# Optimization experiments

Measured on AMD Instinct MI355X. Metric: run time of the kernel, lower is better.

The kernel has to match this reference:

```python
import jax, jax.numpy as jnp
import numpy as np

B, N, H, D, T = 2, 512, 128, 128, 8  # batch, nodes, feat width, mid/out size, triplet fts
Z = 2 * H  # concat(node_fts, hidden)


def _lin_params(key, fan_in, fan_out):
    kw, kb = jax.random.split(key)
    scale = 1.0 / np.sqrt(fan_in)
    w = jax.random.uniform(kw, (fan_in, fan_out), jnp.float32, -scale, scale)
    b = jax.random.uniform(kb, (fan_out,), jnp.float32, -scale, scale)
    return w, b


def setup_inputs() -> dict:
    key = jax.random.key(0)
    ks = jax.random.split(key, 16)
    inp = {
        'node_fts': jax.random.normal(ks[0], (B, N, H), jnp.float32),
        'edge_fts': jax.random.normal(ks[1], (B, N, N, H), jnp.float32),
        'graph_fts': jax.random.normal(ks[2], (B, H), jnp.float32),
        'adj_mat': (jax.random.uniform(ks[3], (B, N, N)) < 0.5).astype(jnp.float32),
        'hidden': jax.random.normal(ks[4], (B, N, H), jnp.float32),
    }
    # message linears
    inp['Wm1'], inp['bm1'] = _lin_params(ks[5], Z, D)
    inp['Wm2'], inp['bm2'] = _lin_params(ks[6], Z, D)
    inp['Wme'], inp['bme'] = _lin_params(ks[7], H, D)
    inp['Wmg'], inp['bmg'] = _lin_params(ks[8], H, D)
    # output linears
    inp['Wo1'], inp['bo1'] = _lin_params(ks[9], Z, D)
    inp['Wo2'], inp['bo2'] = _lin_params(ks[10], D, D)
    # triplet linears
    inp['Wt1'], inp['bt1'] = _lin_params(ks[11], Z, T)
    inp['Wt2'], inp['bt2'] = _lin_params(ks[12], Z, T)
    inp['Wte'], inp['bte'] = _lin_params(ks[13], H, T)
    inp['Wtg'], inp['btg'] = _lin_params(ks[14], H, T)
    return inp


def reference(node_fts, edge_fts, graph_fts, adj_mat, hidden,
              Wm1, bm1, Wm2, bm2, Wme, bme, Wmg, bmg,
              Wo1, bo1, Wo2, bo2,
              Wt1, bt1, Wt2, bt2, Wte, bte, Wtg, btg):
    z = jnp.concatenate([node_fts, hidden], axis=-1)  # [b,n,2h]

    msg_1 = z @ Wm1 + bm1            # [b,n,d]
    msg_2 = z @ Wm2 + bm2            # [b,n,d]
    msg_e = edge_fts @ Wme + bme     # [b,n,n,d]
    msg_g = graph_fts @ Wmg + bmg    # [b,d]

    # triplet messages: broadcast pairwise sum -> relu, shape [b,n,n,t]
    tri = (z @ Wt1 + bt1)[:, None, :, :] \
        + (z @ Wt2 + bt2)[:, :, None, :] \
        + (edge_fts @ Wte + bte) \
        + (graph_fts @ Wtg + btg)[:, None, None, :]
    tri_msgs = jax.nn.relu(tri)

    # pairwise message broadcast-add, mask by adjacency, max over senders (axis 1)
    msgs = msg_1[:, None, :, :] + msg_2[:, :, None, :] + msg_e \
         + msg_g[:, None, None, :]                      # [b,n,n,d]
    msgs = jnp.max(msgs * adj_mat[..., None], axis=1)   # [b,n,d]

    ret = (z @ Wo1 + bo1) + (msgs @ Wo2 + bo2)           # [b,n,d]
    return (ret, tri_msgs)
```

## Files before the change

### kernel.cpp

```cpp
#include <hip/hip_runtime.h>
#include <hip/hip_bf16.h>

#define NB 2
#define NN 512
#define HH 128
#define DD 128
#define TT 8

#define WPACK_OFF 0
#define C_OFF     36864
#define BROW_OFF  561152
#define TC_OFF    1085440
#define TB_OFF    1118208
#define OC_OFF    1150976
#define PART_OFF  1675264
#define ZF_OFF    18452480

#define OUT_TRI   131072

typedef float f32x4 __attribute__((ext_vector_type(4)));
typedef short s16x8 __attribute__((ext_vector_type(8)));

__device__ __forceinline__ unsigned short f2bf(float f) {
    union { float f; unsigned int u; } x; x.f = f;
    unsigned int u = x.u;
    unsigned int r = (u + 0x7FFFu + ((u >> 16) & 1u)) >> 16;
    return (unsigned short)r;
}

__global__ __launch_bounds__(256) void k0_precompute(
    const float* __restrict__ node, const float* __restrict__ hidden,
    const float* __restrict__ graph,
    const float* __restrict__ Wm1, const float* __restrict__ Wm2,
    const float* __restrict__ Wo1, const float* __restrict__ Wmg,
    const float* __restrict__ Wt1, const float* __restrict__ Wt2,
    const float* __restrict__ Wtg,
    const float* __restrict__ Wme, const float* __restrict__ Wte,
    const float* __restrict__ bm1, const float* __restrict__ bm2,
    const float* __restrict__ bme, const float* __restrict__ bmg,
    const float* __restrict__ bo1, const float* __restrict__ bo2,
    const float* __restrict__ bt1, const float* __restrict__ bt2,
    const float* __restrict__ bte, const float* __restrict__ btg,
    char* __restrict__ ws)
{
    const int bx = blockIdx.x, tid = threadIdx.x;
    if (bx == 256) {
        unsigned short* wp = (unsigned short*)(ws + WPACK_OFF);
        for (int idx = tid; idx < 16 * 144 * 8; idx += 256) {
            int j = idx & 7, tmp = idx >> 3;
            int n = tmp % 144, kq = tmp / 144;
            int k = kq * 8 + j;
            float v = 0.f;
            if (n < 128) v = Wme[k * 128 + n];
            else if (n < 136) v = Wte[k * 8 + (n - 128)];
            wp[idx] = f2bf(v);
        }
        return;
    }
    __shared__ float zs[4 * 257];
    const int row0 = bx * 4;
    const int b = row0 >> 9;
    #pragma unroll
    for (int e = 0; e < 4; e++) {
        int idx = e * 256 + tid;
        int rl = idx >> 8, col = idx & 255;
        float v = (col < 128) ? node[(row0 + rl) * 128 + col]
                              : hidden[(row0 + rl) * 128 + col - 128];
        zs[rl * 257 + col] = v;
    }
    __syncthreads();

    float* Cws = (float*)(ws + C_OFF);
    float* Bws = (float*)(ws + BROW_OFF);
    float* Ows = (float*)(ws + OC_OFF);
    float* TCw = (float*)(ws + TC_OFF);
    float* TBw = (float*)(ws + TB_OFF);

    const int d = tid & 127, half = tid >> 7;
    const float* z0 = zs + (half * 2) * 257;
    const float* z1 = zs + (half * 2 + 1) * 257;
    float c0 = 0.f, c1 = 0.f, q0 = 0.f, q1 = 0.f, o0 = 0.f, o1 = 0.f;
    for (int k = 0; k < 256; k++) {
        float w1 = Wm1[k * 128 + d], w2 = Wm2[k * 128 + d], wo = Wo1[k * 128 + d];
        float za = z0[k], zb = z1[k];
        c0 += za * w1; c1 += zb * w1;
        q0 += za * w2; q1 += zb * w2;
        o0 += za * wo; o1 += zb * wo;
    }
    float gm = 0.f;
    for (int k = 0; k < 128; k++) gm += graph[b * 128 + k] * Wmg[k * 128 + d];
    const float cb = gm + bm1[d] + bm2[d] + bme[d] + bmg[d];
    const float ob = bo1[d] + bo2[d];
    const int r0 = row0 + half * 2;
    Cws[r0 * 128 + d] = c0 + cb;  Cws[(r0 + 1) * 128 + d] = c1 + cb;
    Bws[r0 * 128 + d] = q0;       Bws[(r0 + 1) * 128 + d] = q1;
    Ows[r0 * 128 + d] = o0 + ob;  Ows[(r0 + 1) * 128 + d] = o1 + ob;

    if (tid < 64) {
        int r4 = tid >> 4, t = (tid >> 1) & 7, which = tid & 1;
        const float* zr = zs + r4 * 257;
        const float* W = which ? Wt2 : Wt1;
        float acc = 0.f;
        for (int k = 0; k < 256; k++) acc += zr[k] * W[k * 8 + t];
        int rg = row0 + r4;
        if (which == 0) {
            float gt = 0.f;
            for (int k = 0; k < 128; k++) gt += graph[b * 128 + k] * Wtg[k * 8 + t];
            TCw[rg * 8 + t] = acc + gt + bt1[t] + bt2[t] + bte[t] + btg[t];
        } else {
            TBw[rg * 8 + t] = acc;
        }
    }
}

__global__ __launch_bounds__(512, 2) void k2_main(
    const float* __restrict__ edge, const float* __restrict__ adj,
    char* __restrict__ ws, float* __restrict__ out)
{
    __shared__ float red[8][16][64];
    __shared__ int zflag[16];
    const int tid = threadIdx.x;
    const int jt = blockIdx.x, ic = blockIdx.y, b = blockIdx.z;
    const int j0 = jt * 16, i0 = ic * 64;

    const int lane = tid & 63, wave = tid >> 6;
    const int g = wave >> 2, sq = wave & 3;
    const int quad = lane >> 4, l15 = lane & 15;
    const int ntbase = g * 4;

    if (tid < 16) zflag[tid] = 0;
    __syncthreads();

    const float* Bws = (const float*)(ws + BROW_OFF);
    const float* TCw = (const float*)(ws + TC_OFF);
    const float* TBw = (const float*)(ws + TB_OFF);
    const s16x8* wp8 = (const s16x8*)(ws + WPACK_OFF);
    float* part = (float*)(ws + PART_OFF);
    int* Zws = (int*)(ws + ZF_OFF);

    s16x8 Bf[5][4];
    #pragma unroll
    for (int s = 0; s < 4; s++) {
        #pragma unroll
        for (int ntl = 0; ntl < 5; ntl++) {
            int nt = (ntl < 4) ? (ntbase + ntl) : 8;
            Bf[ntl][s] = wp8[(4 * s + quad) * 144 + nt * 16 + l15];
        }
    }

    const int jb = j0 + quad * 4;
    float TCf[4];
    #pragma unroll
    for (int r = 0; r < 4; r++)
        TCf[r] = (l15 < 8) ? TCw[(b * 512 + jb + r) * 8 + l15] : 0.f;

    float Mx[4][4];
    #pragma unroll
    for (int ntl = 0; ntl < 4; ntl++)
        #pragma unroll
        for (int r = 0; r < 4; r++) Mx[ntl][r] = -INFINITY;
    int anyz[4] = {0, 0, 0, 0};

    for (int ii = 0; ii < 16; ii++) {
        const int ig = i0 + sq * 16 + ii;
        const float* erow = edge + ((b * 512 + ig) * 512 + j0 + l15) * 128 + quad * 8;
        s16x8 af[4];
        #pragma unroll
        for (int s = 0; s < 4; s++) {
            float4 p = *(const float4*)(erow + s * 32);
            float4 q = *(const float4*)(erow + s * 32 + 4);
            s16x8 a;
            a[0] = (short)f2bf(p.x); a[1] = (short)f2bf(p.y);
            a[2] = (short)f2bf(p.z); a[3] = (short)f2bf(p.w);
            a[4] = (short)f2bf(q.x); a[5] = (short)f2bf(q.y);
            a[6] = (short)f2bf(q.z); a[7] = (short)f2bf(q.w);
            af[s] = a;
        }
        float adjv[4];
        const int arow = (b * 512 + ig) * 512 + jb;
        #pragma unroll
        for (int r = 0; r < 4; r++) adjv[r] = adj[arow + r];
        float brw[4];
        const int br0 = (b * 512 + ig) * 128;
        #pragma unroll
        for (int ntl = 0; ntl < 4; ntl++)
            brw[ntl] = Bws[br0 + (ntbase + ntl) * 16 + l15];
        const float tb = (l15 < 8) ? TBw[(b * 512 + ig) * 8 + l15] : 0.f;

        f32x4 acc[5];
        #pragma unroll
        for (int ntl = 0; ntl < 5; ntl++) acc[ntl] = (f32x4){0.f, 0.f, 0.f, 0.f};
        #pragma unroll
        for (int s = 0; s < 4; s++) {
            #pragma unroll
            for (int ntl = 0; ntl < 5; ntl++)
                acc[ntl] = __builtin_amdgcn_mfma_f32_16x16x32_bf16(
                    af[s], Bf[ntl][s], acc[ntl], 0, 0, 0);
        }
        #pragma unroll
        for (int r = 0; r < 4; r++) {
            const int isz = (adjv[r] == 0.f);
            anyz[r] |= isz;
            #pragma unroll
            for (int ntl = 0; ntl < 4; ntl++) {
                float v = isz ? -INFINITY : (acc[ntl][r] + brw[ntl]);
                Mx[ntl][r] = fmaxf(Mx[ntl][r], v);
            }
        }
        if (g == 1 && l15 < 8) {
            float* tout = out + OUT_TRI + ((b * 512 + ig) * 512 + jb) * 8 + l15;
            #pragma unroll
            for (int r = 0; r < 4; r++) {
                float tv = acc[4][r] + TCf[r] + tb;
                tout[r * 8] = fmaxf(tv, 0.f);
            }
        }
        if ((ii & 3) == 3) __syncthreads();
    }

    if (g == 0 && l15 == 0) {
        #pragma unroll
        for (int r = 0; r < 4; r++)
            if (anyz[r]) atomicOr(&zflag[quad * 4 + r], 1);
    }
    #pragma unroll
    for (int ntl = 0; ntl < 4; ntl++)
        #pragma unroll
        for (int r = 0; r < 4; r++)
            red[wave][quad * 4 + r][ntl * 16 + l15] = Mx[ntl][r];
    __syncthreads();

    {
        const int q = tid;
        const int j = q >> 5, dq = q & 31;
        const int g2 = dq >> 4, c0 = (dq & 15) * 4;
        const float* r0p = &red[g2 * 4][j][c0];
        float4 m = *(const float4*)r0p;
        #pragma unroll
        for (int w = 1; w < 4; w++) {
            const float4 o = *(const float4*)&red[g2 * 4 + w][j][c0];
            m.x = fmaxf(m.x, o.x); m.y = fmaxf(m.y, o.y);
            m.z = fmaxf(m.z, o.z); m.w = fmaxf(m.w, o.w);
        }
        *(float4*)(part + ((b * 8 + ic) * 512 + j0 + j) * 128 + dq * 4) = m;
    }
    if (tid < 16) Zws[(b * 8 + ic) * 512 + j0 + tid] = zflag[tid];
}

__global__ __launch_bounds__(128) void k3_final(
    const char* __restrict__ ws, const float* __restrict__ Wo2,
    float* __restrict__ out)
{
    __shared__ float ms[128];
    const int bj = blockIdx.x, d = threadIdx.x;
    const int b = bj >> 9, j = bj & 511;
    const float* part = (const float*)(ws + PART_OFF);
    const int* Zws = (const int*)(ws + ZF_OFF);
    const float* Cws = (const float*)(ws + C_OFF);
    const float* Ows = (const float*)(ws + OC_OFF);

    const int rj = b * 512 + j;
    float m = -INFINITY;
    int zf = 0;
    #pragma unroll
    for (int ic = 0; ic < 8; ic++) {
        m = fmaxf(m, part[((b * 8 + ic) * 512 + j) * 128 + d]);
        zf |= Zws[(b * 8 + ic) * 512 + j];
    }
    float c = Cws[rj * 128 + d];
    float mm = fmaxf(m + c, zf ? 0.f : -INFINITY);
    ms[d] = mm;
    __syncthreads();
    float acc = Ows[rj * 128 + d];
    #pragma unroll 8
    for (int k = 0; k < 128; k++) acc += ms[k] * Wo2[k * 128 + d];
    out[rj * 128 + d] = acc;
}

extern "C" void kernel_launch(void* const* d_in, const int* in_sizes, int n_in,
                              void* d_out, int out_size, void* d_ws, size_t ws_size,
                              hipStream_t stream) {
    const float* node   = (const float*)d_in[0];
    const float* edge   = (const float*)d_in[1];
    const float* graph  = (const float*)d_in[2];
    const float* adj    = (const float*)d_in[3];
    const float* hidden = (const float*)d_in[4];
    const float* Wm1 = (const float*)d_in[5];  const float* bm1 = (const float*)d_in[6];
    const float* Wm2 = (const float*)d_in[7];  const float* bm2 = (const float*)d_in[8];
    const float* Wme = (const float*)d_in[9];  const float* bme = (const float*)d_in[10];
    const float* Wmg = (const float*)d_in[11]; const float* bmg = (const float*)d_in[12];
    const float* Wo1 = (const float*)d_in[13]; const float* bo1 = (const float*)d_in[14];
    const float* Wo2 = (const float*)d_in[15]; const float* bo2 = (const float*)d_in[16];
    const float* Wt1 = (const float*)d_in[17]; const float* bt1 = (const float*)d_in[18];
    const float* Wt2 = (const float*)d_in[19]; const float* bt2 = (const float*)d_in[20];
    const float* Wte = (const float*)d_in[21]; const float* bte = (const float*)d_in[22];
    const float* Wtg = (const float*)d_in[23]; const float* btg = (const float*)d_in[24];
    float* out = (float*)d_out;
    char* ws = (char*)d_ws;

    k0_precompute<<<dim3(257), dim3(256), 0, stream>>>(
        node, hidden, graph, Wm1, Wm2, Wo1, Wmg, Wt1, Wt2, Wtg, Wme, Wte,
        bm1, bm2, bme, bmg, bo1, bo2, bt1, bt2, bte, btg, ws);
    k2_main<<<dim3(32, 8, 2), dim3(512), 0, stream>>>(edge, adj, ws, out);
    k3_final<<<dim3(1024), dim3(128), 0, stream>>>(ws, Wo2, out);
}
```

Before: 495.9 us.

## Prefetch next edge row into registers, use packed bf16 convert, drop loop barrier

The main edge loop now loads the next iteration's edge-feature row into registers while the current row is being converted and multiplied, so global load latency overlaps with compute. The float-to-bf16 conversion uses the packed hardware convert builtin when available, falling back to the manual rounding routine otherwise. The periodic __syncthreads inside the loop is removed, letting waves drift apart. The prefetch holds 32 extra floats per thread, which adds register pressure and may lower occupancy.

```diff
diff --git a/kernel.cpp b/kernel.cpp
--- a/kernel.cpp
+++ b/kernel.cpp
@@ -26,6 +26,15 @@
     unsigned int u = x.u;
     unsigned int r = (u + 0x7FFFu + ((u >> 16) & 1u)) >> 16;
     return (unsigned short)r;
+}
+
+__device__ __forceinline__ unsigned cvt2bf(float a, float b) {
+#if __has_builtin(__builtin_amdgcn_cvt_pk_bf16_f32)
+    auto r = __builtin_amdgcn_cvt_pk_bf16_f32(a, b);
+    return __builtin_bit_cast(unsigned, r);
+#else
+    return (unsigned)f2bf(a) | ((unsigned)f2bf(b) << 16);
+#endif
 }
 
 __global__ __launch_bounds__(256) void k0_precompute(
@@ -161,20 +170,36 @@
         for (int r = 0; r < 4; r++) Mx[ntl][r] = -INFINITY;
     int anyz[4] = {0, 0, 0, 0};
 
+    const int ig0 = i0 + sq * 16;
+    const float* erow = edge + ((b * 512 + ig0) * 512 + j0 + l15) * 128 + quad * 8;
+
+    float4 raw[8];
+    #pragma unroll
+    for (int s = 0; s < 4; s++) {
+        raw[2 * s]     = *(const float4*)(erow + s * 32);
+        raw[2 * s + 1] = *(const float4*)(erow + s * 32 + 4);
+    }
+
     for (int ii = 0; ii < 16; ii++) {
-        const int ig = i0 + sq * 16 + ii;
-        const float* erow = edge + ((b * 512 + ig) * 512 + j0 + l15) * 128 + quad * 8;
+        const int ig = ig0 + ii;
         s16x8 af[4];
         #pragma unroll
         for (int s = 0; s < 4; s++) {
-            float4 p = *(const float4*)(erow + s * 32);
-            float4 q = *(const float4*)(erow + s * 32 + 4);
-            s16x8 a;
-            a[0] = (short)f2bf(p.x); a[1] = (short)f2bf(p.y);
-            a[2] = (short)f2bf(p.z); a[3] = (short)f2bf(p.w);
-            a[4] = (short)f2bf(q.x); a[5] = (short)f2bf(q.y);
-            a[6] = (short)f2bf(q.z); a[7] = (short)f2bf(q.w);
-            af[s] = a;
+            union { s16x8 v; unsigned u[4]; } pk;
+            float4 p = raw[2 * s], q = raw[2 * s + 1];
+            pk.u[0] = cvt2bf(p.x, p.y);
+            pk.u[1] = cvt2bf(p.z, p.w);
+            pk.u[2] = cvt2bf(q.x, q.y);
+            pk.u[3] = cvt2bf(q.z, q.w);
+            af[s] = pk.v;
+        }
+        if (ii < 15) {
+            const float* ernx = erow + (ii + 1) * 65536;
+            #pragma unroll
+            for (int s = 0; s < 4; s++) {
+                raw[2 * s]     = *(const float4*)(ernx + s * 32);
+                raw[2 * s + 1] = *(const float4*)(ernx + s * 32 + 4);
+            }
         }
         float adjv[4];
         const int arow = (b * 512 + ig) * 512 + jb;
@@ -215,7 +240,6 @@
                 tout[r * 8] = fmaxf(tv, 0.f);
             }
         }
-        if ((ii & 3) == 3) __syncthreads();
     }
 
     if (g == 0 && l15 == 0) {
```

New measurement: 504.8 us. No clear change (+1.8%).
